# Optimization experiments

Measured on AMD Instinct MI355X. Metric: run time of the kernel, lower is better.

## Reference

```python
import jax, jax.numpy as jnp
import numpy as np
import math

B, S, D, DC, H, L = 8, 4096, 1024, 1024, 16, 2
TOPK, TEMP, MAX_DEPTH, EPS = 2, 1.0, 32, 1e-5

def _gelu(x):
    return jax.nn.gelu(x, approximate=False)

def _ln(x, g=None, b=None):
    mu = x.mean(-1, keepdims=True)
    xc = x - mu
    var = (xc * xc).mean(-1, keepdims=True)
    y = xc * jax.lax.rsqrt(var + EPS)
    if g is not None:
        y = y * g + b
    return y

def setup_inputs() -> dict:
    key = jax.random.key(0)
    ks = iter(jax.random.split(key, 40))
    w = lambda *sh: jax.random.normal(next(ks), sh, dtype=jnp.float32) * 0.02
    inp = {}
    inp['X'] = jax.random.normal(next(ks), (B, S, D), dtype=jnp.float32)
    inp['z'] = jax.random.normal(next(ks), (B, DC), dtype=jnp.float32)
    inp['step_idx'] = 3
    # pool LayerNorm (affine) + input projection
    inp['g_pool'] = jnp.ones((D,)); inp['b_pool'] = jnp.zeros((D,))
    inp['W_inp'] = w(D, DC); inp['b_inp'] = jnp.zeros((DC,))
    # timestep embedding MLP
    inp['Wt1'] = w(DC, 4 * DC); inp['bt1'] = jnp.zeros((4 * DC,))
    inp['Wt2'] = w(4 * DC, DC); inp['bt2'] = jnp.zeros((DC,))
    # cond fusion
    inp['Wc1'] = w(2 * DC, DC); inp['bc1'] = jnp.zeros((DC,))
    inp['Wc2'] = w(DC, DC); inp['bc2'] = jnp.zeros((DC,))
    # denoise blocks (stacked over L)
    inp['W_mod'] = w(L, DC, 4 * DC); inp['b_mod'] = jnp.zeros((L, 4 * DC))
    inp['Wm1'] = w(L, DC, 4 * DC); inp['bm1'] = jnp.zeros((L, 4 * DC))
    inp['Wm2'] = w(L, 4 * DC, DC); inp['bm2'] = jnp.zeros((L, DC))
    # final proj + ln_z
    inp['Wf'] = w(DC, DC); inp['bf'] = jnp.zeros((DC,))
    inp['gz'] = jnp.ones((DC,)); inp['bz'] = jnp.zeros((DC,))
    # router: LN(D+DC) -> Linear -> GELU -> Linear(H)
    inp['gr'] = jnp.ones((D + DC,)); inp['br'] = jnp.zeros((D + DC,))
    inp['Wr1'] = w(D + DC, DC); inp['br1'] = jnp.zeros((DC,))
    inp['Wr2'] = w(DC, H); inp['br2'] = jnp.zeros((H,))
    return inp

def _forward(X, z, step_idx, g_pool, b_pool, W_inp, b_inp, Wt1, bt1, Wt2, bt2,
             Wc1, bc1, Wc2, bc2, W_mod, b_mod, Wm1, bm1, Wm2, bm2,
             Wf, bf, gz, bz, gr, br, Wr1, br1, Wr2, br2):
    # pool tokens -> control vector
    g = _ln(X, g_pool, b_pool).mean(axis=1)            # [B, D]
    x_ctrl = g @ W_inp + b_inp                          # [B, DC]
    # cosine noise schedule, sigma at this depth step
    t = jnp.linspace(0.0, 1.0, MAX_DEPTH)
    sigma_sched = jnp.clip(jnp.cos(t * (math.pi / 2)), 1e-4, None)
    sig = sigma_sched[min(int(step_idx), MAX_DEPTH - 1)]
    # sinusoidal timestep embedding + MLP
    half = DC // 2
    freqs = jnp.exp(-math.log(10000.0) * jnp.arange(half, dtype=jnp.float32) / half)
    args = jnp.broadcast_to(sig * freqs, (B, half))
    emb = jnp.concatenate([jnp.cos(args), jnp.sin(args)], axis=-1)  # [B, DC]
    t_embed = _gelu(emb @ Wt1 + bt1) @ Wt2 + bt2
    # conditioning fusion
    cond = jnp.concatenate([x_ctrl, t_embed], axis=-1)
    cond = _gelu(cond @ Wc1 + bc1) @ Wc2 + bc2          # [B, DC]
    # adaLN denoise blocks
    z_cur = z
    for l in range(L):
        mod = _gelu(cond) @ W_mod[l] + b_mod[l]
        s1, sh1, s2, sh2 = jnp.split(mod, 4, axis=-1)
        h = _ln(z_cur) * (1.0 + s1) + sh1
        h = _gelu(h @ Wm1[l] + bm1[l]) @ Wm2[l] + bm2[l]
        h = h * (1.0 + s2) + sh2
        z_cur = z_cur + h
    z_cur = z_cur @ Wf + bf
    z_cur = _ln(z_cur, gz, bz)                          # [B, DC]
    # token-conditioned router
    zt = jnp.broadcast_to(z_cur[:, None, :], (B, S, DC))
    r = _ln(jnp.concatenate([X, zt], axis=-1), gr, br)  # [B, S, D+DC]
    logits = _gelu(r @ Wr1 + br1) @ Wr2 + br2           # [B, S, H]
    alpha = jax.nn.softmax(logits / TEMP, axis=-1)
    # top-k mask + renormalize
    topv, topi = jax.lax.top_k(alpha, TOPK)
    bi = jnp.arange(B)[:, None, None]
    si = jnp.arange(S)[None, :, None]
    masked = jnp.zeros_like(alpha).at[bi, si, topi].set(topv)
    denom = jnp.maximum(masked.sum(axis=-1, keepdims=True), 1e-12)
    return masked / denom                               # [B, S, H]

def reference(X, z, step_idx, g_pool, b_pool, W_inp, b_inp, Wt1, bt1, Wt2, bt2,
              Wc1, bc1, Wc2, bc2, W_mod, b_mod, Wm1, bm1, Wm2, bm2,
              Wf, bf, gz, bz, gr, br, Wr1, br1, Wr2, br2):
    return _forward(X, z, step_idx, g_pool, b_pool, W_inp, b_inp, Wt1, bt1, Wt2, bt2,
                    Wc1, bc1, Wc2, bc2, W_mod, b_mod, Wm1, bm1, Wm2, bm2,
                    Wf, bf, gz, bz, gr, br, Wr1, br1, Wr2, br2)
```

## Files before the change

kernel.cpp:

```cpp
#include <hip/hip_runtime.h>
#include <cstdint>
#include <cstddef>
#include <math.h>

#define DEV __device__ __forceinline__


typedef short s8v __attribute__((ext_vector_type(8)));
typedef float f4v __attribute__((ext_vector_type(4)));

DEV float geluf(float x) { return 0.5f * x * (1.0f + erff(x * 0.70710678118654752440f)); }
DEV double gelud(double x) { return 0.5 * x * (1.0 + erf(x * 0.70710678118654752440)); }
DEV unsigned short f2us(float f) {
    unsigned u = __float_as_uint(f);
    u += 0x7fffu + ((u >> 16) & 1u);
    return (unsigned short)(u >> 16);
}

DEV void gload16(const void* g, void* l) {
    __builtin_amdgcn_global_load_lds(
        (const __attribute__((address_space(1))) void*)g,
        (__attribute__((address_space(3))) void*)l, 16, 0, 0);
}

DEV void blockReduce2d(double& a, double& b, double* lds ) {
    __syncthreads();
#pragma unroll
    for (int off = 32; off >= 1; off >>= 1) {
        a += __shfl_xor(a, off, 64);
        b += __shfl_xor(b, off, 64);
    }
    int w = threadIdx.x >> 6;
    if ((threadIdx.x & 63) == 0) { lds[w] = a; lds[4 + w] = b; }
    __syncthreads();
    a = lds[0] + lds[1] + lds[2] + lds[3];
    b = lds[4] + lds[5] + lds[6] + lds[7];
    __syncthreads();
}

__global__ __launch_bounds__(256) void pool_kernel(
    const float* __restrict__ X, double* __restrict__ Macc,
    double* __restrict__ tokstats,
    unsigned short* __restrict__ XH, unsigned short* __restrict__ XL)
{
    int b = blockIdx.y;
    int w = threadIdx.x >> 6, l = threadIdx.x & 63;
    int s0 = blockIdx.x * 64 + w * 16;
    double acc[16];
#pragma unroll
    for (int e = 0; e < 16; e++) acc[e] = 0.0;
    __shared__ double red[4][1024];

    for (int t = 0; t < 16; t++) {
        int s = s0 + t;
        const float* row = X + (size_t)(b * 4096 + s) * 1024;
        float xv[16];
#pragma unroll
        for (int m = 0; m < 16; m++) xv[m] = row[l + 64 * m];
        if (XH) {
            size_t base = (size_t)(b * 4096 + s) * 1024 + l;
#pragma unroll
            for (int m = 0; m < 16; m++) {
                unsigned u = __float_as_uint(xv[m]);
                XH[base + 64 * m] = (unsigned short)(u >> 16);
                float r = xv[m] - __uint_as_float(u & 0xffff0000u);
                XL[base + 64 * m] = (unsigned short)(__float_as_uint(r) >> 16);
            }
        }
        double s1 = 0.0, s2 = 0.0;
#pragma unroll
        for (int m = 0; m < 16; m++) { double x = (double)xv[m]; s1 += x; s2 += x * x; }
#pragma unroll
        for (int off = 32; off >= 1; off >>= 1) {
            s1 += __shfl_xor(s1, off, 64);
            s2 += __shfl_xor(s2, off, 64);
        }
        double mu = s1 * (1.0 / 1024.0);
        double var = s2 * (1.0 / 1024.0) - mu * mu;
        double istd = 1.0 / sqrt(var + 1e-5);
        if (l == 0) {
            tokstats[(size_t)(b * 4096 + s) * 2]     = s1;
            tokstats[(size_t)(b * 4096 + s) * 2 + 1] = s2;
        }
#pragma unroll
        for (int m = 0; m < 16; m++) acc[m] += ((double)xv[m] - mu) * istd;
    }
#pragma unroll
    for (int m = 0; m < 16; m++) red[w][l + 64 * m] = acc[m];
    __syncthreads();
    for (int d = threadIdx.x; d < 1024; d += 256)
        atomicAdd(&Macc[b * 1024 + d], red[0][d] + red[1][d] + red[2][d] + red[3][d]);
}

__global__ void prep_kernel(const int* __restrict__ step_idx,
                            const float* __restrict__ z,
                            double* __restrict__ emb, double* __restrict__ z0)
{
    int step = step_idx[0];
    if (step > 31) step = 31;
    double t = (double)step / 31.0;
    double sig = cos(t * 1.5707963267948966);
    if (sig < 1e-4) sig = 1e-4;
    for (int k = threadIdx.x; k < 512; k += 256) {
        double fr = exp(-9.210340371976184 * ((double)k / 512.0));
        double a = sig * fr;
        emb[k] = cos(a);
        emb[512 + k] = sin(a);
    }
    for (int i = threadIdx.x; i < 8192; i += 256) z0[i] = (double)z[i];
}

__global__ __launch_bounds__(256) void prepw_kernel(
    const float* __restrict__ Wr1, const float* __restrict__ gr,
    unsigned short* __restrict__ WThi, unsigned short* __restrict__ WTlo)
{
    __shared__ unsigned short th[64][65], tl[64][65];
    int tx = threadIdx.x & 63, ty = threadIdx.x >> 6;
    int i0 = blockIdx.y * 64, j0 = blockIdx.x * 64;
#pragma unroll 4
    for (int k = 0; k < 16; k++) {
        int row = ty * 16 + k;
        float w = (float)((double)gr[i0 + row] * (double)Wr1[(size_t)(i0 + row) * 1024 + j0 + tx]);
        unsigned short hi = f2us(w);
        float hif = __uint_as_float((unsigned)hi << 16);
        unsigned short lo = f2us(w - hif);
        th[row][tx] = hi;
        tl[row][tx] = lo;
    }
    __syncthreads();
#pragma unroll 4
    for (int k = 0; k < 16; k++) {
        int row = ty * 16 + k;
        WThi[(size_t)(j0 + row) * 1024 + i0 + tx] = th[tx][row];
        WTlo[(size_t)(j0 + row) * 1024 + i0 + tx] = tl[tx][row];
    }
}

__global__ __launch_bounds__(256) void colsum_kernel(
    const float* __restrict__ Wr1, const float* __restrict__ gr,
    const float* __restrict__ br, const float* __restrict__ br1,
    double* __restrict__ Cvec, double* __restrict__ hbvec)
{
    int j = blockIdx.x * 256 + threadIdx.x;
    int i0 = blockIdx.y * 128;
    double c = 0.0, bw = 0.0;
#pragma unroll 4
    for (int k = 0; k < 128; k++) {
        int i = i0 + k;
        double wv = (double)Wr1[(size_t)i * 1024 + j];
        c += (double)gr[i] * wv;
        bw += (double)br[i] * wv;
    }
    if (blockIdx.y == 0) bw += (double)br1[j];
    atomicAdd(&Cvec[j], c);
    atomicAdd(&hbvec[j], bw);
}

template <int IN, int R>
__global__ __launch_bounds__(256) void gemvd_kernel(
    const float* __restrict__ W, int K, int N, int kchunk, int kstr,
    const double* __restrict__ in0, const double* __restrict__ in1,
    const double* __restrict__ in2,
    const float* __restrict__ ba0, const float* __restrict__ ba1,
    double* __restrict__ out)
{
    const int CH = 64;
    __shared__ double xin[R][CH];
    int tid = threadIdx.x;
    int j = blockIdx.x * 256 + tid;
    int kbeg = blockIdx.y * kchunk;
    double acc[R];
#pragma unroll
    for (int r = 0; r < R; r++) acc[r] = 0.0;

    for (int k0 = kbeg; k0 < kbeg + kchunk; k0 += CH) {
        for (int idx = tid; idx < R * CH; idx += 256) {
            int r = idx / CH, ii = idx % CH, i = k0 + ii;
            double v;
            if (IN == 0) {
                v = in0[(size_t)r * kstr + i] + (ba0 ? (double)ba0[i] : 0.0);
            } else if (IN == 1) {
                v = (double)ba0[i] * (in0[(size_t)r * kstr + i] * (1.0 / 4096.0)) + (double)ba1[i];
            } else if (IN == 2) {
                v = gelud(in0[(size_t)r * kstr + i] + (ba0 ? (double)ba0[i] : 0.0));
            } else if (IN == 3) {
                double mu = in1[r * 2], istd = in1[r * 2 + 1];
                double s1 = in2[(size_t)r * 4096 + i] + (double)ba0[i];
                double sh1 = in2[(size_t)r * 4096 + 1024 + i] + (double)ba0[1024 + i];
                v = (in0[(size_t)r * 1024 + i] - mu) * istd * (1.0 + s1) + sh1;
            } else {
                v = (i < 1024) ? (in0[(size_t)r * 1024 + i] + (double)ba0[i])
                               : (in1[i - 1024] + (double)ba1[i - 1024]);
            }
            xin[r][ii] = v;
        }
        __syncthreads();
#pragma unroll 16
        for (int kk = 0; kk < CH; kk++) {
            double wv = (double)W[(size_t)(k0 + kk) * N + j];
#pragma unroll
            for (int r = 0; r < R; r++) acc[r] += xin[r][kk] * wv;
        }
        __syncthreads();
    }
#pragma unroll
    for (int r = 0; r < R; r++) atomicAdd(&out[(size_t)r * N + j], acc[r]);
}

__global__ void stats8_kernel(const double* __restrict__ z, double* __restrict__ zstats)
{
    __shared__ double lds[8];
    int r = blockIdx.x, tid = threadIdx.x;
    double s = 0.0, ss = 0.0;
    for (int i = tid; i < 1024; i += 256) {
        double v = z[(size_t)r * 1024 + i];
        s += v; ss += v * v;
    }
    blockReduce2d(s, ss, lds);
    if (tid == 0) {
        double mu = s * (1.0 / 1024.0);
        double var = ss * (1.0 / 1024.0) - mu * mu;
        zstats[r * 2] = mu;
        zstats[r * 2 + 1] = 1.0 / sqrt(var + 1e-5);
    }
}

__global__ void resid_kernel(const double* __restrict__ zc, const double* __restrict__ h2pre,
                             const float* __restrict__ bm2,
                             const double* __restrict__ modpre,
                             const float* __restrict__ bmod,
                             double* __restrict__ znew, double* __restrict__ zstats)
{
    __shared__ double lds[8];
    int r = blockIdx.x, tid = threadIdx.x;
    double s = 0.0, ss = 0.0;
#pragma unroll
    for (int c = 0; c < 4; c++) {
        int i = tid + c * 256;
        double s2 = modpre[(size_t)r * 4096 + 2048 + i] + (double)bmod[2048 + i];
        double sh2 = modpre[(size_t)r * 4096 + 3072 + i] + (double)bmod[3072 + i];
        double h = h2pre[(size_t)r * 1024 + i] + (double)bm2[i];
        double v = zc[(size_t)r * 1024 + i] + h * (1.0 + s2) + sh2;
        znew[(size_t)r * 1024 + i] = v;
        s += v; ss += v * v;
    }
    blockReduce2d(s, ss, lds);
    if (tid == 0) {
        double mu = s * (1.0 / 1024.0);
        double var = ss * (1.0 / 1024.0) - mu * mu;
        zstats[r * 2] = mu;
        zstats[r * 2 + 1] = 1.0 / sqrt(var + 1e-5);
    }
}

__global__ void zfinal_kernel(const double* __restrict__ zfpre,
                              const float* __restrict__ bfb,
                              const float* __restrict__ gz,
                              const float* __restrict__ bz,
                              const float* __restrict__ gr,
                              double* __restrict__ zv, double* __restrict__ zrstats)
{
    __shared__ double xb[1024];
    __shared__ double lds[8];
    int r = blockIdx.x, tid = threadIdx.x;
    double s = 0.0, ss = 0.0;
#pragma unroll
    for (int c = 0; c < 4; c++) {
        int i = tid + c * 256;
        double x = zfpre[(size_t)r * 1024 + i] + (double)bfb[i];
        xb[i] = x;
        s += x; ss += x * x;
    }
    blockReduce2d(s, ss, lds);
    double mu = s * (1.0 / 1024.0);
    double var = ss * (1.0 / 1024.0) - mu * mu;
    double istd = 1.0 / sqrt(var + 1e-5);
    double s2 = 0.0, s2s = 0.0;
#pragma unroll
    for (int c = 0; c < 4; c++) {
        int i = tid + c * 256;
        double zf = (xb[i] - mu) * istd * (double)gz[i] + (double)bz[i];
        zv[(size_t)r * 1024 + i] = zf * (double)gr[1024 + i];
        s2 += zf; s2s += zf * zf;
    }
    blockReduce2d(s2, s2s, lds);
    if (tid == 0) { zrstats[r * 2] = s2; zrstats[r * 2 + 1] = s2s; }
}

__global__ __launch_bounds__(256) void router2_kernel(
    const unsigned short* __restrict__ XH, const unsigned short* __restrict__ XL,
    const unsigned short* __restrict__ WThi, const unsigned short* __restrict__ WTlo,
    const double* __restrict__ tokstats, const double* __restrict__ zrstats,
    const double* __restrict__ Vmat, const double* __restrict__ Cvec,
    const double* __restrict__ hbvec, const float* __restrict__ Wr2,
    float* __restrict__ logits)
{
    __shared__ struct {
        union {
            struct { unsigned short Ah[128 * 32], Al[128 * 32],
                                    Bh[128 * 32], Bl[128 * 32]; } g;
            struct { float Ht[64 * 133]; float W2[1024]; } e;
        } u;
        float mus[128], iss[128], Vs[128], Cs[128], hbs[128];
    } sm;

    const int tid = threadIdx.x;
    const int id = blockIdx.x;
    const int xcd = id & 7, local = id >> 3;
    const int tokTile = xcd * 32 + (local >> 3);
    const int nTile = local & 7;
    const int n0 = nTile * 128, tok0 = tokTile * 128;
    const int b = tok0 >> 12;

    if (tid < 128) {
        int tok = tok0 + tid;
        double mu = (tokstats[(size_t)tok * 2] + zrstats[b * 2]) * (1.0 / 2048.0);
        double var = (tokstats[(size_t)tok * 2 + 1] + zrstats[b * 2 + 1]) * (1.0 / 2048.0) - mu * mu;
        sm.mus[tid] = (float)mu;
        sm.iss[tid] = (float)(1.0 / sqrt(var + 1e-5));
    } else {
        int n = tid - 128;
        sm.Vs[n] = (float)Vmat[(size_t)b * 1024 + n0 + n];
        sm.Cs[n] = (float)Cvec[n0 + n];
        sm.hbs[n] = (float)hbvec[n0 + n];
    }

    const int l = tid & 63, wid = tid >> 6;
    const int wm = wid >> 1, wn = wid & 1;
    const int lr = l & 15, q = l >> 4;

    const unsigned short* gS[8]; char* lS[8];
    {
        const unsigned short* srcs[4] = {
            XH + (size_t)tok0 * 1024, XL + (size_t)tok0 * 1024,
            WThi + (size_t)n0 * 1024, WTlo + (size_t)n0 * 1024 };
        char* dsts[4] = { (char*)sm.u.g.Ah, (char*)sm.u.g.Al,
                          (char*)sm.u.g.Bh, (char*)sm.u.g.Bl };
#pragma unroll
        for (int s = 0; s < 4; s++)
#pragma unroll
            for (int it = 0; it < 2; it++) {
                int c = it * 256 + tid;
                int m = c >> 2, p = (c & 3) ^ ((m >> 1) & 3);
                gS[s * 2 + it] = srcs[s] + (size_t)m * 1024 + p * 8;
                lS[s * 2 + it] = dsts[s] + c * 16;
            }
    }

    int aoff[4], boff[4];
#pragma unroll
    for (int i = 0; i < 4; i++) {
        int ra = wm * 64 + i * 16 + lr;
        aoff[i] = ra * 32 + ((q ^ ((ra >> 1) & 3)) << 3);
        int rb = wn * 64 + i * 16 + lr;
        boff[i] = rb * 32 + ((q ^ ((rb >> 1) & 3)) << 3);
    }

    f4v acc[4][4];
#pragma unroll
    for (int mi = 0; mi < 4; mi++)
#pragma unroll
        for (int ni = 0; ni < 4; ni++) acc[mi][ni] = (f4v){0.f, 0.f, 0.f, 0.f};

    for (int k0 = 0; k0 < 1024; k0 += 32) {
#pragma unroll
        for (int t = 0; t < 8; t++) gload16(gS[t] + k0, lS[t]);
        __syncthreads();

        s8v ah[4], al[4], bh4[4], bl4[4];
#pragma unroll
        for (int i = 0; i < 4; i++) {
            ah[i]  = *(const s8v*)(sm.u.g.Ah + aoff[i]);
            al[i]  = *(const s8v*)(sm.u.g.Al + aoff[i]);
            bh4[i] = *(const s8v*)(sm.u.g.Bh + boff[i]);
            bl4[i] = *(const s8v*)(sm.u.g.Bl + boff[i]);
        }
#pragma unroll
        for (int mi = 0; mi < 4; mi++)
#pragma unroll
            for (int ni = 0; ni < 4; ni++) {
                acc[mi][ni] = __builtin_amdgcn_mfma_f32_16x16x32_bf16(ah[mi], bh4[ni], acc[mi][ni], 0, 0, 0);
                acc[mi][ni] = __builtin_amdgcn_mfma_f32_16x16x32_bf16(al[mi], bh4[ni], acc[mi][ni], 0, 0, 0);
                acc[mi][ni] = __builtin_amdgcn_mfma_f32_16x16x32_bf16(ah[mi], bl4[ni], acc[mi][ni], 0, 0, 0);
            }
        __syncthreads();
    }

    float lacc[8];
#pragma unroll
    for (int h = 0; h < 8; h++) lacc[h] = 0.f;
    const int g2 = tid >> 7, mrow = tid & 127;

#pragma unroll
    for (int p = 0; p < 2; p++) {
#pragma unroll
        for (int nh = 0; nh < 2; nh++) {
            int ni = 2 * p + nh;
            int n = wn * 64 + ni * 16 + lr;
            int jl = wn * 32 + nh * 16 + lr;
            float Vn = sm.Vs[n], Cn = sm.Cs[n], hbn = sm.hbs[n];
#pragma unroll
            for (int mi = 0; mi < 4; mi++) {
#pragma unroll
                for (int rr = 0; rr < 4; rr++) {
                    int m = wm * 64 + mi * 16 + q * 4 + rr;
                    float h = sm.iss[m] * (acc[mi][ni][rr] + Vn - sm.mus[m] * Cn) + hbn;
                    sm.u.e.Ht[jl * 133 + m] = geluf(h);
                }
            }
        }
        for (int idx = tid; idx < 1024; idx += 256) {
            int jl = idx >> 4;
            int n = ((jl >> 5) << 6) + p * 32 + (jl & 31);
            sm.u.e.W2[idx] = Wr2[(size_t)(n0 + n) * 16 + (idx & 15)];
        }
        __syncthreads();
#pragma unroll 8
        for (int jl = 0; jl < 64; jl++) {
            float x = sm.u.e.Ht[jl * 133 + mrow];
#pragma unroll
            for (int h = 0; h < 8; h++) lacc[h] += x * sm.u.e.W2[jl * 16 + g2 * 8 + h];
        }
        __syncthreads();
    }
#pragma unroll
    for (int h = 0; h < 8; h++)
        atomicAdd(&logits[(size_t)(tok0 + mrow) * 16 + g2 * 8 + h], lacc[h]);
}

__global__ __launch_bounds__(256) void router_kernel(
    const float* __restrict__ X, const unsigned short* __restrict__ WThi,
    const unsigned short* __restrict__ WTlo,
    const double* __restrict__ tokstats, const double* __restrict__ zrstats,
    const double* __restrict__ Vmat, const double* __restrict__ Cvec,
    const double* __restrict__ hbvec, const float* __restrict__ Wr2,
    float* __restrict__ logits)
{
    __shared__ struct {
        union {
            struct { float Af[128 * 32]; unsigned short Bh[128 * 32]; unsigned short Bl[128 * 32]; } g;
            struct { float Ht[64 * 133]; float W2[1024]; } e;
        } u;
        float mus[128], iss[128], Vs[128], Cs[128], hbs[128];
    } sm;

    const int tid = threadIdx.x;
    const int n0 = blockIdx.x * 128, tok0 = blockIdx.y * 128;
    const int b = tok0 >> 12;

    if (tid < 128) {
        int tok = tok0 + tid;
        double mu = (tokstats[(size_t)tok * 2] + zrstats[b * 2]) * (1.0 / 2048.0);
        double var = (tokstats[(size_t)tok * 2 + 1] + zrstats[b * 2 + 1]) * (1.0 / 2048.0) - mu * mu;
        sm.mus[tid] = (float)mu;
        sm.iss[tid] = (float)(1.0 / sqrt(var + 1e-5));
    } else {
        int n = tid - 128;
        sm.Vs[n] = (float)Vmat[(size_t)b * 1024 + n0 + n];
        sm.Cs[n] = (float)Cvec[n0 + n];
        sm.hbs[n] = (float)hbvec[n0 + n];
    }

    const int l = tid & 63, wid = tid >> 6;
    const int wm = wid >> 1, wn = wid & 1;
    const int lr = l & 15, q = l >> 4;

    const float* gA[4]; char* lA[4];
#pragma unroll
    for (int it = 0; it < 4; it++) {
        int c = it * 256 + tid;
        int m = c >> 3;
        int pg = (c & 7) ^ (m & 7);
        gA[it] = X + (size_t)(tok0 + m) * 1024 + pg * 4;
        lA[it] = (char*)sm.u.g.Af + c * 16;
    }
    const unsigned short *gBh[2], *gBl[2];
    char *lBh[2], *lBl[2];
#pragma unroll
    for (int it = 0; it < 2; it++) {
        int c = it * 256 + tid;
        int m = c >> 2;
        int p = (c & 3) ^ ((m >> 1) & 3);
        gBh[it] = WThi + (size_t)(n0 + m) * 1024 + p * 8;
        gBl[it] = WTlo + (size_t)(n0 + m) * 1024 + p * 8;
        lBh[it] = (char*)sm.u.g.Bh + c * 16;
        lBl[it] = (char*)sm.u.g.Bl + c * 16;
    }

    int boff[4], aoffr[4], s7a[4];
#pragma unroll
    for (int i = 0; i < 4; i++) {
        int rb = wn * 64 + i * 16 + lr;
        boff[i] = rb * 32 + ((q ^ ((rb >> 1) & 3)) << 3);
        int ra = wm * 64 + i * 16 + lr;
        aoffr[i] = ra * 32;
        s7a[i] = ra & 7;
    }

    f4v acc[4][4];
#pragma unroll
    for (int mi = 0; mi < 4; mi++)
#pragma unroll
        for (int ni = 0; ni < 4; ni++) acc[mi][ni] = (f4v){0.f, 0.f, 0.f, 0.f};

    for (int k0 = 0; k0 < 1024; k0 += 32) {
#pragma unroll
        for (int it = 0; it < 4; it++) gload16(gA[it] + k0, lA[it]);
#pragma unroll
        for (int it = 0; it < 2; it++) {
            gload16(gBh[it] + k0, lBh[it]);
            gload16(gBl[it] + k0, lBl[it]);
        }
        __syncthreads();

        s8v ah[4], al[4], bh4[4], bl4[4];
#pragma unroll
        for (int i = 0; i < 4; i++) {
            const float* Ab = sm.u.g.Af + aoffr[i];
            float4 f0 = *(const float4*)(Ab + ((((2 * q))     ^ s7a[i]) << 2));
            float4 f1 = *(const float4*)(Ab + ((((2 * q) | 1) ^ s7a[i]) << 2));
            unsigned u0 = __float_as_uint(f0.x), u1 = __float_as_uint(f0.y),
                     u2 = __float_as_uint(f0.z), u3 = __float_as_uint(f0.w),
                     u4 = __float_as_uint(f1.x), u5 = __float_as_uint(f1.y),
                     u6 = __float_as_uint(f1.z), u7 = __float_as_uint(f1.w);
            int4 hi4, lo4;
            hi4.x = (int)((u0 >> 16) | (u1 & 0xffff0000u));
            hi4.y = (int)((u2 >> 16) | (u3 & 0xffff0000u));
            hi4.z = (int)((u4 >> 16) | (u5 & 0xffff0000u));
            hi4.w = (int)((u6 >> 16) | (u7 & 0xffff0000u));
            float r0 = f0.x - __uint_as_float(u0 & 0xffff0000u);
            float r1 = f0.y - __uint_as_float(u1 & 0xffff0000u);
            float r2 = f0.z - __uint_as_float(u2 & 0xffff0000u);
            float r3 = f0.w - __uint_as_float(u3 & 0xffff0000u);
            float r4 = f1.x - __uint_as_float(u4 & 0xffff0000u);
            float r5 = f1.y - __uint_as_float(u5 & 0xffff0000u);
            float r6 = f1.z - __uint_as_float(u6 & 0xffff0000u);
            float r7 = f1.w - __uint_as_float(u7 & 0xffff0000u);
            lo4.x = (int)((__float_as_uint(r0) >> 16) | (__float_as_uint(r1) & 0xffff0000u));
            lo4.y = (int)((__float_as_uint(r2) >> 16) | (__float_as_uint(r3) & 0xffff0000u));
            lo4.z = (int)((__float_as_uint(r4) >> 16) | (__float_as_uint(r5) & 0xffff0000u));
            lo4.w = (int)((__float_as_uint(r6) >> 16) | (__float_as_uint(r7) & 0xffff0000u));
            ah[i] = __builtin_bit_cast(s8v, hi4);
            al[i] = __builtin_bit_cast(s8v, lo4);
            bh4[i] = *(const s8v*)(sm.u.g.Bh + boff[i]);
            bl4[i] = *(const s8v*)(sm.u.g.Bl + boff[i]);
        }
#pragma unroll
        for (int mi = 0; mi < 4; mi++)
#pragma unroll
            for (int ni = 0; ni < 4; ni++) {
                acc[mi][ni] = __builtin_amdgcn_mfma_f32_16x16x32_bf16(ah[mi], bh4[ni], acc[mi][ni], 0, 0, 0);
                acc[mi][ni] = __builtin_amdgcn_mfma_f32_16x16x32_bf16(al[mi], bh4[ni], acc[mi][ni], 0, 0, 0);
                acc[mi][ni] = __builtin_amdgcn_mfma_f32_16x16x32_bf16(ah[mi], bl4[ni], acc[mi][ni], 0, 0, 0);
            }
        __syncthreads();
    }

    float lacc[8];
#pragma unroll
    for (int h = 0; h < 8; h++) lacc[h] = 0.f;
    const int g2 = tid >> 7, mrow = tid & 127;

#pragma unroll
    for (int p = 0; p < 2; p++) {
#pragma unroll
        for (int nh = 0; nh < 2; nh++) {
            int ni = 2 * p + nh;
            int n = wn * 64 + ni * 16 + lr;
            int jl = wn * 32 + nh * 16 + lr;
            float Vn = sm.Vs[n], Cn = sm.Cs[n], hbn = sm.hbs[n];
#pragma unroll
            for (int mi = 0; mi < 4; mi++) {
#pragma unroll
                for (int rr = 0; rr < 4; rr++) {
                    int m = wm * 64 + mi * 16 + q * 4 + rr;
                    float h = sm.iss[m] * (acc[mi][ni][rr] + Vn - sm.mus[m] * Cn) + hbn;
                    sm.u.e.Ht[jl * 133 + m] = geluf(h);
                }
            }
        }
        for (int idx = tid; idx < 1024; idx += 256) {
            int jl = idx >> 4;
            int n = ((jl >> 5) << 6) + p * 32 + (jl & 31);
            sm.u.e.W2[idx] = Wr2[(size_t)(n0 + n) * 16 + (idx & 15)];
        }
        __syncthreads();
#pragma unroll 8
        for (int jl = 0; jl < 64; jl++) {
            float x = sm.u.e.Ht[jl * 133 + mrow];
#pragma unroll
            for (int h = 0; h < 8; h++) lacc[h] += x * sm.u.e.W2[jl * 16 + g2 * 8 + h];
        }
        __syncthreads();
    }
#pragma unroll
    for (int h = 0; h < 8; h++)
        atomicAdd(&logits[(size_t)(tok0 + mrow) * 16 + g2 * 8 + h], lacc[h]);
}

#define FLAG_CAP 16384
__global__ __launch_bounds__(256) void softflag_kernel(
    const float* __restrict__ logits, const float* __restrict__ br2,
    float* __restrict__ out, int* __restrict__ cnt, int* __restrict__ flagged)
{
    int t = blockIdx.x * 256 + threadIdx.x;
    float v[16];
    const float4* lp = (const float4*)(logits + (size_t)t * 16);
    float4 a0 = lp[0], a1 = lp[1], a2 = lp[2], a3 = lp[3];
    v[0] = a0.x; v[1] = a0.y; v[2] = a0.z; v[3] = a0.w;
    v[4] = a1.x; v[5] = a1.y; v[6] = a1.z; v[7] = a1.w;
    v[8] = a2.x; v[9] = a2.y; v[10] = a2.z; v[11] = a2.w;
    v[12] = a3.x; v[13] = a3.y; v[14] = a3.z; v[15] = a3.w;
#pragma unroll
    for (int h = 0; h < 16; h++) v[h] += br2[h];
    int i1 = 0; float b1 = v[0];
#pragma unroll
    for (int h = 1; h < 16; h++) if (v[h] > b1) { b1 = v[h]; i1 = h; }
    int i2 = -1; float b2 = -3.4e38f;
#pragma unroll
    for (int h = 0; h < 16; h++) if (h != i1 && v[h] > b2) { b2 = v[h]; i2 = h; }
    float b3 = -3.4e38f;
#pragma unroll
    for (int h = 0; h < 16; h++) if (h != i1 && h != i2 && v[h] > b3) b3 = v[h];
    float mx = b1;
    float e1 = expf(b1 - mx), e2 = expf(b2 - mx);
    float s = 0.f;
#pragma unroll
    for (int h = 0; h < 16; h++) s += expf(v[h] - mx);
    float a1v = e1 / s, a2v = e2 / s;
    float den = fmaxf(a1v + a2v, 1e-12f);
    float r1 = a1v / den, r2 = a2v / den;
    float o[16];
#pragma unroll
    for (int h = 0; h < 16; h++) o[h] = (h == i1 ? r1 : (h == i2 ? r2 : 0.f));
    float4* op = (float4*)(out + (size_t)t * 16);
    op[0] = make_float4(o[0], o[1], o[2], o[3]);
    op[1] = make_float4(o[4], o[5], o[6], o[7]);
    op[2] = make_float4(o[8], o[9], o[10], o[11]);
    op[3] = make_float4(o[12], o[13], o[14], o[15]);
    if (b2 - b3 < 1e-3f) {
        int slot = atomicAdd(cnt, 1);
        if (slot < FLAG_CAP) flagged[slot] = t;
    }
}

__global__ void flagstat_kernel(const float* __restrict__ X,
                                const double* __restrict__ zrstats,
                                const int* __restrict__ cnt,
                                const int* __restrict__ flagged,
                                double* __restrict__ fstats)
{
    int n = cnt[0]; if (n > FLAG_CAP) n = FLAG_CAP;
    int s = blockIdx.x;
    if (s >= n) return;
    int tok = flagged[s], b = tok >> 12;
    int l = threadIdx.x;
    double s1 = 0.0, s2 = 0.0;
#pragma unroll
    for (int m = 0; m < 16; m++) {
        double x = (double)X[(size_t)tok * 1024 + l + 64 * m];
        s1 += x; s2 += x * x;
    }
#pragma unroll
    for (int off = 32; off >= 1; off >>= 1) {
        s1 += __shfl_xor(s1, off, 64);
        s2 += __shfl_xor(s2, off, 64);
    }
    if (l == 0) {
        double mu = (s1 + zrstats[b * 2]) * (1.0 / 2048.0);
        double var = (s2 + zrstats[b * 2 + 1]) * (1.0 / 2048.0) - mu * mu;
        fstats[s * 2] = mu;
        fstats[s * 2 + 1] = 1.0 / sqrt(var + 1e-5);
    }
}

__global__ __launch_bounds__(256) void exact2_kernel(
    const float* __restrict__ X, const float* __restrict__ Wr1,
    const float* __restrict__ gr, const double* __restrict__ zv,
    const double* __restrict__ Cvec, const double* __restrict__ hbvec,
    const float* __restrict__ Wr2,
    const int* __restrict__ cnt, const int* __restrict__ flagged,
    const double* __restrict__ fstats, double* __restrict__ exlog)
{
    int n = cnt[0]; if (n > FLAG_CAP) n = FLAG_CAP;
    const int c = blockIdx.y;
    if (c * 16 >= n) return;
    int nt = n - c * 16; if (nt > 16) nt = 16;

    __shared__ double aS[16][65];
    __shared__ double gS[16][129];
    __shared__ double mus[16], iss[16];
    __shared__ int toks[16];

    const int tid = threadIdx.x;
    const int j0 = blockIdx.x * 128;
    const int jl = tid & 127;
    const int j = j0 + jl;
    const int tg = (tid >> 7) * 8;

    if (tid < 16) {
        if (tid < nt) {
            toks[tid] = flagged[c * 16 + tid];
            mus[tid] = fstats[(size_t)(c * 16 + tid) * 2];
            iss[tid] = fstats[(size_t)(c * 16 + tid) * 2 + 1];
        } else {
            toks[tid] = 0; mus[tid] = 0.0; iss[tid] = 0.0;
        }
    }
    __syncthreads();

    double acc[8];
#pragma unroll
    for (int t = 0; t < 8; t++) acc[t] = 0.0;

    for (int i0 = 0; i0 < 2048; i0 += 64) {
        for (int idx = tid; idx < 1024; idx += 256) {
            int t = idx >> 6, ii = idx & 63, i = i0 + ii;
            double v = 0.0;
            if (t < nt) {
                int tok = toks[t];
                if (i < 1024)
                    v = (double)X[(size_t)tok * 1024 + i] * (double)gr[i];
                else
                    v = zv[(size_t)(tok >> 12) * 1024 + (i - 1024)];
            }
            aS[t][ii] = v;
        }
        __syncthreads();
#pragma unroll 8
        for (int ii = 0; ii < 64; ii++) {
            double wv = (double)Wr1[(size_t)(i0 + ii) * 1024 + j];
#pragma unroll
            for (int t = 0; t < 8; t++) acc[t] += aS[tg + t][ii] * wv;
        }
        __syncthreads();
    }

    {
        double Cj = Cvec[j], hbj = hbvec[j];
#pragma unroll
        for (int t = 0; t < 8; t++) {
            double pre = iss[tg + t] * (acc[t] - mus[tg + t] * Cj) + hbj;
            gS[tg + t][jl] = gelud(pre);
        }
    }
    __syncthreads();

    {
        int t = tid >> 4, h = tid & 15;
        double p = 0.0;
#pragma unroll 8
        for (int j2 = 0; j2 < 128; j2++)
            p += gS[t][j2] * (double)Wr2[(size_t)(j0 + j2) * 16 + h];
        if (t < nt)
            atomicAdd(&exlog[(size_t)(c * 16 + t) * 16 + h], p);
    }
}

__global__ __launch_bounds__(256) void fix_kernel(
    const double* __restrict__ exlog, const float* __restrict__ br2,
    const int* __restrict__ cnt, const int* __restrict__ flagged,
    float* __restrict__ out)
{
    int s = blockIdx.x * 256 + threadIdx.x;
    int n = cnt[0]; if (n > FLAG_CAP) n = FLAG_CAP;
    if (s >= n) return;
    int tok = flagged[s];
    double v[16];
#pragma unroll
    for (int h = 0; h < 16; h++) v[h] = exlog[(size_t)s * 16 + h] + (double)br2[h];
    int i1 = 0; double b1 = v[0];
#pragma unroll
    for (int h = 1; h < 16; h++) if (v[h] > b1) { b1 = v[h]; i1 = h; }
    int i2 = -1; double b2 = -1e300;
#pragma unroll
    for (int h = 0; h < 16; h++) if (h != i1 && v[h] > b2) { b2 = v[h]; i2 = h; }
    double ssum = 0.0;
#pragma unroll
    for (int h = 0; h < 16; h++) ssum += exp(v[h] - b1);
    double a1v = exp(b1 - b1) / ssum, a2v = exp(b2 - b1) / ssum;
    double den = a1v + a2v; if (den < 1e-12) den = 1e-12;
    float r1 = (float)(a1v / den), r2 = (float)(a2v / den);
#pragma unroll
    for (int h = 0; h < 16; h++)
        out[(size_t)tok * 16 + h] = (h == i1 ? r1 : (h == i2 ? r2 : 0.f));
}

extern "C" void kernel_launch(void* const* d_in, const int* in_sizes, int n_in,
                              void* d_out, int out_size, void* d_ws, size_t ws_size,
                              hipStream_t stream)
{
    const float* X      = (const float*)d_in[0];
    const float* z_in   = (const float*)d_in[1];
    const int*   stepi  = (const int*)d_in[2];
    const float* g_pool = (const float*)d_in[3];
    const float* b_pool = (const float*)d_in[4];
    const float* W_inp  = (const float*)d_in[5];
    const float* b_inp  = (const float*)d_in[6];
    const float* Wt1    = (const float*)d_in[7];
    const float* bt1    = (const float*)d_in[8];
    const float* Wt2    = (const float*)d_in[9];
    const float* bt2    = (const float*)d_in[10];
    const float* Wc1    = (const float*)d_in[11];
    const float* bc1    = (const float*)d_in[12];
    const float* Wc2    = (const float*)d_in[13];
    const float* bc2    = (const float*)d_in[14];
    const float* W_mod  = (const float*)d_in[15];
    const float* b_mod  = (const float*)d_in[16];
    const float* Wm1    = (const float*)d_in[17];
    const float* bm1    = (const float*)d_in[18];
    const float* Wm2    = (const float*)d_in[19];
    const float* bm2    = (const float*)d_in[20];
    const float* Wf     = (const float*)d_in[21];
    const float* bf_b   = (const float*)d_in[22];
    const float* gz     = (const float*)d_in[23];
    const float* bz     = (const float*)d_in[24];
    const float* gr     = (const float*)d_in[25];
    const float* br     = (const float*)d_in[26];
    const float* Wr1    = (const float*)d_in[27];
    const float* br1    = (const float*)d_in[28];
    const float* Wr2    = (const float*)d_in[29];
    const float* br2    = (const float*)d_in[30];

    char* wsb = (char*)d_ws;
    const size_t OB_LOGA  = 0;
    const size_t OB_EXLOG = 2097152;
    const size_t OB_CNT   = 4194304;
    const size_t OB_FLAG  = 4194368;
    const size_t OB_MACC  = 4259904;
    const size_t OB_XCTRL = 4325440;
    const size_t OB_TH1   = 4390976;
    const size_t OB_TEMB  = 4423744;
    const size_t OB_CH    = 4431936;
    const size_t OB_COND  = 4497472;
    const size_t OB_MOD   = 4563008;
    const size_t OB_H1    = 5087296;
    const size_t OB_H2    = 5611584;
    const size_t OB_ZFPRE = 5742656;
    const size_t OB_V     = 5808192;
    const size_t OB_TOKST = 5873728;
    const size_t OB_FSTAT = 6398016;
    const size_t OB_EMB   = 6660160;
    const size_t OB_ZB0   = 6668352;
    const size_t OB_ZB1   = 6733888;
    const size_t OB_ZST   = 6799424;
    const size_t OB_ZRST  = 6799552;
    const size_t OB_ZV    = 6799680;
    const size_t OB_CVEC  = 6865216;
    const size_t OB_HB    = 6873408;
    const size_t ZEND     = 6881600;
    const size_t OB_WTHI  = 6881600;
    const size_t OB_WTLO  = 8978752;
    const size_t OB_XH    = 11075904;
    const size_t OB_XL    = 78184768;
    const size_t WS_BIG   = 145293632;

    unsigned short* WThi = (unsigned short*)(wsb + OB_WTHI);
    unsigned short* WTlo = (unsigned short*)(wsb + OB_WTLO);
    int* cntp  = (int*)(wsb + OB_CNT);
    int* flagp = (int*)(wsb + OB_FLAG);

    const bool big = ws_size >= WS_BIG;
    unsigned short* XHp = big ? (unsigned short*)(wsb + OB_XH) : nullptr;
    unsigned short* XLp = big ? (unsigned short*)(wsb + OB_XL) : nullptr;

    hipMemsetAsync(d_ws, 0, ZEND, stream);

    pool_kernel<<<dim3(64, 8), 256, 0, stream>>>(X, (double*)(wsb + OB_MACC),
                                                 (double*)(wsb + OB_TOKST), XHp, XLp);
    prep_kernel<<<1, 256, 0, stream>>>(stepi, z_in, (double*)(wsb + OB_EMB), (double*)(wsb + OB_ZB0));
    prepw_kernel<<<dim3(16, 16), 256, 0, stream>>>(Wr1, gr, WThi, WTlo);
    colsum_kernel<<<dim3(4, 16), 256, 0, stream>>>(Wr1, gr, br, br1,
        (double*)(wsb + OB_CVEC), (double*)(wsb + OB_HB));

    gemvd_kernel<1, 8><<<dim3(4, 16), 256, 0, stream>>>(W_inp, 1024, 1024, 64, 1024,
        (double*)(wsb + OB_MACC), nullptr, nullptr, g_pool, b_pool, (double*)(wsb + OB_XCTRL));
    gemvd_kernel<0, 1><<<dim3(16, 16), 256, 0, stream>>>(Wt1, 1024, 4096, 64, 1024,
        (double*)(wsb + OB_EMB), nullptr, nullptr, nullptr, nullptr, (double*)(wsb + OB_TH1));
    gemvd_kernel<2, 1><<<dim3(4, 16), 256, 0, stream>>>(Wt2, 4096, 1024, 256, 4096,
        (double*)(wsb + OB_TH1), nullptr, nullptr, bt1, nullptr, (double*)(wsb + OB_TEMB));
    gemvd_kernel<4, 8><<<dim3(4, 16), 256, 0, stream>>>(Wc1, 2048, 1024, 128, 1024,
        (double*)(wsb + OB_XCTRL), (double*)(wsb + OB_TEMB), nullptr, b_inp, bt2, (double*)(wsb + OB_CH));
    gemvd_kernel<2, 8><<<dim3(4, 16), 256, 0, stream>>>(Wc2, 1024, 1024, 64, 1024,
        (double*)(wsb + OB_CH), nullptr, nullptr, bc1, nullptr, (double*)(wsb + OB_COND));

    stats8_kernel<<<8, 256, 0, stream>>>((double*)(wsb + OB_ZB0), (double*)(wsb + OB_ZST));

    for (int ll = 0; ll < 2; ll++) {
        double* zcur  = (double*)(wsb + (ll == 0 ? OB_ZB0 : OB_ZB1));
        double* znext = (double*)(wsb + (ll == 0 ? OB_ZB1 : OB_ZB0));
        double* modp  = (double*)(wsb + OB_MOD) + (size_t)ll * 32768;
        double* h1p   = (double*)(wsb + OB_H1) + (size_t)ll * 32768;
        double* h2p   = (double*)(wsb + OB_H2) + (size_t)ll * 8192;
        gemvd_kernel<2, 8><<<dim3(16, 16), 256, 0, stream>>>(W_mod + (size_t)ll * 4194304,
            1024, 4096, 64, 1024, (double*)(wsb + OB_COND), nullptr, nullptr, bc2, nullptr, modp);
        gemvd_kernel<3, 8><<<dim3(16, 16), 256, 0, stream>>>(Wm1 + (size_t)ll * 4194304,
            1024, 4096, 64, 1024, zcur, (double*)(wsb + OB_ZST), modp, b_mod + ll * 4096, nullptr, h1p);
        gemvd_kernel<2, 8><<<dim3(4, 16), 256, 0, stream>>>(Wm2 + (size_t)ll * 4194304,
            4096, 1024, 256, 4096, h1p, nullptr, nullptr, bm1 + ll * 4096, nullptr, h2p);
        resid_kernel<<<8, 256, 0, stream>>>(zcur, h2p, bm2 + ll * 1024, modp,
                                            b_mod + ll * 4096, znext, (double*)(wsb + OB_ZST));
    }

    gemvd_kernel<0, 8><<<dim3(4, 16), 256, 0, stream>>>(Wf, 1024, 1024, 64, 1024,
        (double*)(wsb + OB_ZB0), nullptr, nullptr, nullptr, nullptr, (double*)(wsb + OB_ZFPRE));
    zfinal_kernel<<<8, 256, 0, stream>>>((double*)(wsb + OB_ZFPRE), bf_b, gz, bz, gr,
                                         (double*)(wsb + OB_ZV), (double*)(wsb + OB_ZRST));
    gemvd_kernel<0, 8><<<dim3(4, 16), 256, 0, stream>>>(Wr1 + (size_t)1024 * 1024,
        1024, 1024, 64, 1024, (double*)(wsb + OB_ZV), nullptr, nullptr, nullptr, nullptr,
        (double*)(wsb + OB_V));

    if (big) {
        router2_kernel<<<2048, 256, 0, stream>>>(XHp, XLp, WThi, WTlo,
            (double*)(wsb + OB_TOKST), (double*)(wsb + OB_ZRST), (double*)(wsb + OB_V),
            (double*)(wsb + OB_CVEC), (double*)(wsb + OB_HB), Wr2, (float*)(wsb + OB_LOGA));
    } else {
        router_kernel<<<dim3(8, 256), 256, 0, stream>>>(X, WThi, WTlo,
            (double*)(wsb + OB_TOKST), (double*)(wsb + OB_ZRST), (double*)(wsb + OB_V),
            (double*)(wsb + OB_CVEC), (double*)(wsb + OB_HB), Wr2, (float*)(wsb + OB_LOGA));
    }

    softflag_kernel<<<128, 256, 0, stream>>>((float*)(wsb + OB_LOGA), br2,
        (float*)d_out, cntp, flagp);
    flagstat_kernel<<<16384, 64, 0, stream>>>(X, (double*)(wsb + OB_ZRST), cntp, flagp,
        (double*)(wsb + OB_FSTAT));
    exact2_kernel<<<dim3(8, 1024), 256, 0, stream>>>(X, Wr1, gr, (double*)(wsb + OB_ZV),
        (double*)(wsb + OB_CVEC), (double*)(wsb + OB_HB), Wr2, cntp, flagp,
        (double*)(wsb + OB_FSTAT), (double*)(wsb + OB_EXLOG));
    fix_kernel<<<64, 256, 0, stream>>>((double*)(wsb + OB_EXLOG), br2, cntp, flagp,
        (float*)d_out);
}
```

Baseline: 1.729 ms.

## Double-buffer hi tiles in LDS and load lo tiles directly from global

The router GEMM kernel now keeps only the bf16 hi halves of X and the weight tile in LDS, double-buffered so the next k-slice loads while the current one is computed, which leaves one barrier per iteration. The lo halves are read straight from global memory into registers. LayerNorm stats and bias vectors move from shared memory into registers, and the epilogue handles 16-column chunks to shrink LDS use. The goal is to hide load latency and free LDS so more blocks fit per CU. The cost is uncoalesced, uncached-in-LDS global reads for the lo operands and more register pressure.

```diff
diff --git a/kernel.cpp b/kernel.cpp
--- a/kernel.cpp
+++ b/kernel.cpp
@@ -287,7 +287,7 @@
     if (tid == 0) { zrstats[r * 2] = s2; zrstats[r * 2 + 1] = s2s; }
 }
 
-__global__ __launch_bounds__(256) void router2_kernel(
+__global__ __launch_bounds__(256) void router3_kernel(
     const unsigned short* __restrict__ XH, const unsigned short* __restrict__ XL,
     const unsigned short* __restrict__ WThi, const unsigned short* __restrict__ WTlo,
     const double* __restrict__ tokstats, const double* __restrict__ zrstats,
@@ -295,13 +295,9 @@
     const double* __restrict__ hbvec, const float* __restrict__ Wr2,
     float* __restrict__ logits)
 {
-    __shared__ struct {
-        union {
-            struct { unsigned short Ah[128 * 32], Al[128 * 32],
-                                    Bh[128 * 32], Bl[128 * 32]; } g;
-            struct { float Ht[64 * 133]; float W2[1024]; } e;
-        } u;
-        float mus[128], iss[128], Vs[128], Cs[128], hbs[128];
+    __shared__ union {
+        unsigned short hb[16384];
+        struct { float Ht[32 * 133]; float W2[512]; } e;
     } sm;
 
     const int tid = threadIdx.x;
@@ -312,48 +308,31 @@
     const int n0 = nTile * 128, tok0 = tokTile * 128;
     const int b = tok0 >> 12;
 
-    if (tid < 128) {
-        int tok = tok0 + tid;
-        double mu = (tokstats[(size_t)tok * 2] + zrstats[b * 2]) * (1.0 / 2048.0);
-        double var = (tokstats[(size_t)tok * 2 + 1] + zrstats[b * 2 + 1]) * (1.0 / 2048.0) - mu * mu;
-        sm.mus[tid] = (float)mu;
-        sm.iss[tid] = (float)(1.0 / sqrt(var + 1e-5));
-    } else {
-        int n = tid - 128;
-        sm.Vs[n] = (float)Vmat[(size_t)b * 1024 + n0 + n];
-        sm.Cs[n] = (float)Cvec[n0 + n];
-        sm.hbs[n] = (float)hbvec[n0 + n];
-    }
-
     const int l = tid & 63, wid = tid >> 6;
     const int wm = wid >> 1, wn = wid & 1;
     const int lr = l & 15, q = l >> 4;
 
-    const unsigned short* gS[8]; char* lS[8];
-    {
-        const unsigned short* srcs[4] = {
-            XH + (size_t)tok0 * 1024, XL + (size_t)tok0 * 1024,
-            WThi + (size_t)n0 * 1024, WTlo + (size_t)n0 * 1024 };
-        char* dsts[4] = { (char*)sm.u.g.Ah, (char*)sm.u.g.Al,
-                          (char*)sm.u.g.Bh, (char*)sm.u.g.Bl };
-#pragma unroll
-        for (int s = 0; s < 4; s++)
-#pragma unroll
-            for (int it = 0; it < 2; it++) {
-                int c = it * 256 + tid;
-                int m = c >> 2, p = (c & 3) ^ ((m >> 1) & 3);
-                gS[s * 2 + it] = srcs[s] + (size_t)m * 1024 + p * 8;
-                lS[s * 2 + it] = dsts[s] + c * 16;
-            }
+    const unsigned short *gA[2], *gB[2];
+    int ldst[2];
+#pragma unroll
+    for (int it = 0; it < 2; it++) {
+        int c = it * 256 + tid;
+        int m = c >> 2, p = (c & 3) ^ ((m >> 1) & 3);
+        gA[it] = XH + (size_t)(tok0 + m) * 1024 + p * 8;
+        gB[it] = WThi + (size_t)(n0 + m) * 1024 + p * 8;
+        ldst[it] = c * 16;
     }
 
     int aoff[4], boff[4];
+    const unsigned short *pAlo[4], *pBlo[4];
 #pragma unroll
     for (int i = 0; i < 4; i++) {
         int ra = wm * 64 + i * 16 + lr;
         aoff[i] = ra * 32 + ((q ^ ((ra >> 1) & 3)) << 3);
         int rb = wn * 64 + i * 16 + lr;
         boff[i] = rb * 32 + ((q ^ ((rb >> 1) & 3)) << 3);
+        pAlo[i] = XL + (size_t)(tok0 + ra) * 1024 + q * 8;
+        pBlo[i] = WTlo + (size_t)(n0 + rb) * 1024 + q * 8;
     }
 
     f4v acc[4][4];
@@ -362,28 +341,78 @@
 #pragma unroll
         for (int ni = 0; ni < 4; ni++) acc[mi][ni] = (f4v){0.f, 0.f, 0.f, 0.f};
 
+    char* hbase = (char*)sm.hb;
+#pragma unroll
+    for (int it = 0; it < 2; it++) {
+        gload16(gA[it], hbase + ldst[it]);
+        gload16(gB[it], hbase + 16384 + ldst[it]);
+    }
+    __syncthreads();
+
+    int cur = 0;
     for (int k0 = 0; k0 < 1024; k0 += 32) {
-#pragma unroll
-        for (int t = 0; t < 8; t++) gload16(gS[t] + k0, lS[t]);
-        __syncthreads();
-
-        s8v ah[4], al[4], bh4[4], bl4[4];
+        if (k0 + 32 < 1024) {
+            int nxt = cur ^ 1;
+#pragma unroll
+            for (int it = 0; it < 2; it++) {
+                gload16(gA[it] + k0 + 32, hbase + nxt * 8192 + ldst[it]);
+                gload16(gB[it] + k0 + 32, hbase + 16384 + nxt * 8192 + ldst[it]);
+            }
+        }
+        s8v alv[4], blv[4], ah[4], bh4[4];
 #pragma unroll
         for (int i = 0; i < 4; i++) {
-            ah[i]  = *(const s8v*)(sm.u.g.Ah + aoff[i]);
-            al[i]  = *(const s8v*)(sm.u.g.Al + aoff[i]);
-            bh4[i] = *(const s8v*)(sm.u.g.Bh + boff[i]);
-            bl4[i] = *(const s8v*)(sm.u.g.Bl + boff[i]);
+            alv[i] = *(const s8v*)(pAlo[i] + k0);
+            blv[i] = *(const s8v*)(pBlo[i] + k0);
+        }
+        const unsigned short* Abuf = sm.hb + cur * 4096;
+        const unsigned short* Bbuf = sm.hb + 8192 + cur * 4096;
+#pragma unroll
+        for (int i = 0; i < 4; i++) {
+            ah[i]  = *(const s8v*)(Abuf + aoff[i]);
+            bh4[i] = *(const s8v*)(Bbuf + boff[i]);
         }
 #pragma unroll
         for (int mi = 0; mi < 4; mi++)
 #pragma unroll
-            for (int ni = 0; ni < 4; ni++) {
+            for (int ni = 0; ni < 4; ni++)
                 acc[mi][ni] = __builtin_amdgcn_mfma_f32_16x16x32_bf16(ah[mi], bh4[ni], acc[mi][ni], 0, 0, 0);
-                acc[mi][ni] = __builtin_amdgcn_mfma_f32_16x16x32_bf16(al[mi], bh4[ni], acc[mi][ni], 0, 0, 0);
-                acc[mi][ni] = __builtin_amdgcn_mfma_f32_16x16x32_bf16(ah[mi], bl4[ni], acc[mi][ni], 0, 0, 0);
+#pragma unroll
+        for (int mi = 0; mi < 4; mi++)
+#pragma unroll
+            for (int ni = 0; ni < 4; ni++)
+                acc[mi][ni] = __builtin_amdgcn_mfma_f32_16x16x32_bf16(alv[mi], bh4[ni], acc[mi][ni], 0, 0, 0);
+#pragma unroll
+        for (int mi = 0; mi < 4; mi++)
+#pragma unroll
+            for (int ni = 0; ni < 4; ni++)
+                acc[mi][ni] = __builtin_amdgcn_mfma_f32_16x16x32_bf16(ah[mi], blv[ni], acc[mi][ni], 0, 0, 0);
+        __syncthreads();
+        cur ^= 1;
+    }
+
+    float mus_r[4][4], iss_r[4][4];
+    {
+        double zr1 = zrstats[b * 2], zr2 = zrstats[b * 2 + 1];
+#pragma unroll
+        for (int mi = 0; mi < 4; mi++)
+#pragma unroll
+            for (int rr = 0; rr < 4; rr++) {
+                int m = wm * 64 + mi * 16 + q * 4 + rr;
+                size_t tok = (size_t)(tok0 + m);
+                double mu = (tokstats[tok * 2] + zr1) * (1.0 / 2048.0);
+                double var = (tokstats[tok * 2 + 1] + zr2) * (1.0 / 2048.0) - mu * mu;
+                mus_r[mi][rr] = (float)mu;
+                iss_r[mi][rr] = (float)(1.0 / sqrt(var + 1e-5));
             }
-        __syncthreads();
+    }
+    float Vn[4], Cn[4], hbn[4];
+#pragma unroll
+    for (int ni = 0; ni < 4; ni++) {
+        int n = wn * 64 + ni * 16 + lr;
+        Vn[ni]  = (float)Vmat[(size_t)b * 1024 + n0 + n];
+        Cn[ni]  = (float)Cvec[n0 + n];
+        hbn[ni] = (float)hbvec[n0 + n];
     }
 
     float lacc[8];
@@ -392,34 +421,28 @@
     const int g2 = tid >> 7, mrow = tid & 127;
 
 #pragma unroll
-    for (int p = 0; p < 2; p++) {
-#pragma unroll
-        for (int nh = 0; nh < 2; nh++) {
-            int ni = 2 * p + nh;
-            int n = wn * 64 + ni * 16 + lr;
-            int jl = wn * 32 + nh * 16 + lr;
-            float Vn = sm.Vs[n], Cn = sm.Cs[n], hbn = sm.hbs[n];
-#pragma unroll
-            for (int mi = 0; mi < 4; mi++) {
-#pragma unroll
-                for (int rr = 0; rr < 4; rr++) {
-                    int m = wm * 64 + mi * 16 + q * 4 + rr;
-                    float h = sm.iss[m] * (acc[mi][ni][rr] + Vn - sm.mus[m] * Cn) + hbn;
-                    sm.u.e.Ht[jl * 133 + m] = geluf(h);
-                }
+    for (int p2 = 0; p2 < 4; p2++) {
+        int jl = wn * 16 + lr;
+#pragma unroll
+        for (int mi = 0; mi < 4; mi++) {
+#pragma unroll
+            for (int rr = 0; rr < 4; rr++) {
+                int m = wm * 64 + mi * 16 + q * 4 + rr;
+                float h = iss_r[mi][rr] * (acc[mi][p2][rr] + Vn[p2] - mus_r[mi][rr] * Cn[p2]) + hbn[p2];
+                sm.e.Ht[jl * 133 + m] = geluf(h);
             }
         }
-        for (int idx = tid; idx < 1024; idx += 256) {
-            int jl = idx >> 4;
-            int n = ((jl >> 5) << 6) + p * 32 + (jl & 31);
-            sm.u.e.W2[idx] = Wr2[(size_t)(n0 + n) * 16 + (idx & 15)];
+        for (int idx = tid; idx < 512; idx += 256) {
+            int j2 = idx >> 4;
+            int n = ((j2 >> 4) << 6) + p2 * 16 + (j2 & 15);
+            sm.e.W2[idx] = Wr2[(size_t)(n0 + n) * 16 + (idx & 15)];
         }
         __syncthreads();
 #pragma unroll 8
-        for (int jl = 0; jl < 64; jl++) {
-            float x = sm.u.e.Ht[jl * 133 + mrow];
-#pragma unroll
-            for (int h = 0; h < 8; h++) lacc[h] += x * sm.u.e.W2[jl * 16 + g2 * 8 + h];
+        for (int j2 = 0; j2 < 32; j2++) {
+            float x = sm.e.Ht[j2 * 133 + mrow];
+#pragma unroll
+            for (int h = 0; h < 8; h++) lacc[h] += x * sm.e.W2[j2 * 16 + g2 * 8 + h];
         }
         __syncthreads();
     }
@@ -568,13 +591,13 @@
             int ni = 2 * p + nh;
             int n = wn * 64 + ni * 16 + lr;
             int jl = wn * 32 + nh * 16 + lr;
-            float Vn = sm.Vs[n], Cn = sm.Cs[n], hbn = sm.hbs[n];
+            float Vnx = sm.Vs[n], Cnx = sm.Cs[n], hbnx = sm.hbs[n];
 #pragma unroll
             for (int mi = 0; mi < 4; mi++) {
 #pragma unroll
                 for (int rr = 0; rr < 4; rr++) {
                     int m = wm * 64 + mi * 16 + q * 4 + rr;
-                    float h = sm.iss[m] * (acc[mi][ni][rr] + Vn - sm.mus[m] * Cn) + hbn;
+                    float h = sm.iss[m] * (acc[mi][ni][rr] + Vnx - sm.mus[m] * Cnx) + hbnx;
                     sm.u.e.Ht[jl * 133 + m] = geluf(h);
                 }
             }
@@ -911,7 +934,7 @@
         (double*)(wsb + OB_V));
 
     if (big) {
-        router2_kernel<<<2048, 256, 0, stream>>>(XHp, XLp, WThi, WTlo,
+        router3_kernel<<<2048, 256, 0, stream>>>(XHp, XLp, WThi, WTlo,
             (double*)(wsb + OB_TOKST), (double*)(wsb + OB_ZRST), (double*)(wsb + OB_V),
             (double*)(wsb + OB_CVEC), (double*)(wsb + OB_HB), Wr2, (float*)(wsb + OB_LOGA));
     } else {
```

Measured after the change: 1.758 ms. No clear change (+1.6%).
